# Performance work log

Hardware: AMD Instinct MI355X
Metric: run time of the kernel (lower is better)

The kernel has to match this reference:

```python
import jax, jax.numpy as jnp
import numpy as np
from jax import lax


def _layernorm(x, g, b, eps=1e-5):
    m = x.mean(-1, keepdims=True)
    v = ((x - m) ** 2).mean(-1, keepdims=True)
    return (x - m) * lax.rsqrt(v + eps) * g + b


def _conv1d(x, w, b):
    # x: (B, T, Cin), w: (K, Cin, Cout) -> SAME padding (kernel=3, pad=1)
    y = lax.conv_general_dilated(x, w, (1,), 'SAME',
                                 dimension_numbers=('NWC', 'WIO', 'NWC'))
    return y + b


def _predictor(x, params, mask):
    w1, b1, g1, be1, w2, b2, g2, be2, wl, bl = params
    h = _layernorm(jax.nn.relu(_conv1d(x, w1, b1)), g1, be1)
    h = _layernorm(jax.nn.relu(_conv1d(h, w2, b2)), g2, be2)
    out = (h @ wl)[..., 0] + bl[0]          # (B, T)
    return jnp.where(mask, 0.0, out)


def _length_regulate(x, dur, max_len):
    # vectorized equivalent of the per-token expand/cat/pad loop
    cum = jnp.cumsum(dur, axis=1)            # (B, S)
    mel_len = cum[:, -1]                     # (B,)
    pos = jnp.arange(max_len)                # (T,)
    idx = jax.vmap(lambda c: jnp.searchsorted(c, pos, side='right'))(cum)
    idx = jnp.minimum(idx, x.shape[1] - 1)   # (B, T)
    out = jnp.take_along_axis(x, idx[:, :, None], axis=1)
    valid = (pos[None, :] < mel_len[:, None])[:, :, None]
    return jnp.where(valid, out, 0.0), mel_len


def setup_inputs() -> dict:
    key = jax.random.key(0)
    ks = jax.random.split(key, 12)
    B, S, D, F, K, T, NB = 32, 512, 512, 512, 3, 4096, 256
    inp = {
        'x': jax.random.normal(ks[0], (B, S, D), jnp.float32),
        'src_mask': jnp.zeros((B, S), bool),
        'mel_mask': jnp.zeros((B, T), bool),
        'pitch_truth': jax.random.normal(ks[1], (B, S), jnp.float32),
        'energy_truth': jax.random.normal(ks[2], (B, S), jnp.float32),
        'duration_truth': jax.random.randint(ks[3], (B, S), 0, 8, jnp.int32),
        'conv1_w': 0.05 * jax.random.normal(ks[4], (3, K, D, F), jnp.float32),
        'conv1_b': jnp.zeros((3, F), jnp.float32),
        'ln1_g': jnp.ones((3, F), jnp.float32),
        'ln1_b': jnp.zeros((3, F), jnp.float32),
        'conv2_w': 0.05 * jax.random.normal(ks[5], (3, K, F, F), jnp.float32),
        'conv2_b': jnp.zeros((3, F), jnp.float32),
        'ln2_g': jnp.ones((3, F), jnp.float32),
        'ln2_b': jnp.zeros((3, F), jnp.float32),
        'lin_w': 0.05 * jax.random.normal(ks[6], (3, F, 1), jnp.float32),
        'lin_b': jnp.zeros((3, 1), jnp.float32),
        'pitch_emb': 0.05 * jax.random.normal(ks[7], (NB, D), jnp.float32),
        'energy_emb': 0.05 * jax.random.normal(ks[8], (NB, D), jnp.float32),
        'pitch_bins': jnp.linspace(-3.0, 3.0, NB - 1),
        'energy_bins': jnp.linspace(-3.0, 3.0, NB - 1),
        'max_mel_len': T,
    }
    return inp


def reference(x, src_mask, mel_mask, pitch_truth, energy_truth, duration_truth,
              conv1_w, conv1_b, ln1_g, ln1_b, conv2_w, conv2_b, ln2_g, ln2_b,
              lin_w, lin_b, pitch_emb, energy_emb, pitch_bins, energy_bins,
              max_mel_len):
    def params(i):
        return (conv1_w[i], conv1_b[i], ln1_g[i], ln1_b[i],
                conv2_w[i], conv2_b[i], ln2_g[i], ln2_b[i], lin_w[i], lin_b[i])

    # pitch (predictor idx 0)
    pitch_pred = _predictor(x, params(0), src_mask)
    x = x + pitch_emb[jnp.searchsorted(pitch_bins, pitch_truth, side='left')]
    # energy (idx 1)
    energy_pred = _predictor(x, params(1), src_mask)
    x = x + energy_emb[jnp.searchsorted(energy_bins, energy_truth, side='left')]
    # duration (idx 2)
    log_dur = _predictor(x, params(2), src_mask)
    # length regulation with ground-truth durations (training path)
    x_out, mel_len = _length_regulate(x, duration_truth, max_mel_len)
    return x_out, pitch_pred, energy_pred, log_dur, mel_len, mel_mask
```

## Files before the change

### kernel.cpp

```cpp
#include <hip/hip_runtime.h>
#include <hip/hip_bf16.h>


#define B_ 32
#define S_ 512
#define D_ 512
#define F_ 512
#define T_ 4096
#define SP_ 514
#define KK_ 1536
#define NITER 12
#define SLOT ((size_t)B_ * SP_ * D_)

typedef __attribute__((ext_vector_type(8))) short bf16x8;
typedef __attribute__((ext_vector_type(4))) float f32x4;

__device__ __forceinline__ float bf2f(unsigned short u) {
  union { unsigned int i; float f; } c; c.i = (unsigned int)u << 16; return c.f;
}
__device__ __forceinline__ unsigned short f2bf(float f) {
  __hip_bfloat16 h = __float2bfloat16(f);
  return *(unsigned short*)&h;
}

struct Job {
  const __hip_bfloat16* Pin;
  const __hip_bfloat16* WT;
  const float* bias;
  const float* g;
  const float* be;
  const float* wl;
  const float* bl;
  const unsigned char* mask;
  __hip_bfloat16* Pout;
  float* pred;
  int mode;
};

#define WT_BLKS 1152
#define TP_BLKS 8224
__global__ __launch_bounds__(256) void prep_k(const float* __restrict__ x,
                                              const float* __restrict__ W1,
                                              const float* __restrict__ W2,
                                              const int* __restrict__ dur,
                                              const float* __restrict__ ptruth,
                                              const float* __restrict__ pbins,
                                              const float* __restrict__ pemb,
                                              const float* __restrict__ etruth,
                                              const float* __restrict__ ebins,
                                              const float* __restrict__ eemb,
                                              __hip_bfloat16* __restrict__ X0,
                                              __hip_bfloat16* __restrict__ X1,
                                              __hip_bfloat16* __restrict__ X2,
                                              __hip_bfloat16* __restrict__ P0,
                                              __hip_bfloat16* __restrict__ P1,
                                              __hip_bfloat16* __restrict__ WT1,
                                              __hip_bfloat16* __restrict__ WT2,
                                              int* __restrict__ cum,
                                              float* __restrict__ mel_len) {
  const int blk = blockIdx.x;
  const int t = threadIdx.x;
  if (blk < WT_BLKS) {
    __shared__ float tb[64][65];
    const int w = blk / 192;
    const int kt = (blk % 192) >> 3;
    const int ft = blk & 7;
    const float* src = (w < 3) ? (W1 + (size_t)w * KK_ * F_)
                               : (W2 + (size_t)(w - 3) * KK_ * F_);
    __hip_bfloat16* dst = (w < 3) ? (WT1 + (size_t)w * KK_ * F_)
                                  : (WT2 + (size_t)(w - 3) * KK_ * F_);
    const int ty = t >> 4, tx = t & 15;
    #pragma unroll
    for (int j = 0; j < 4; ++j) {
      const int r = ty + j * 16;
      const float4 v = *(const float4*)(src + (size_t)(kt * 64 + r) * F_ + ft * 64 + tx * 4);
      tb[r][tx * 4 + 0] = v.x; tb[r][tx * 4 + 1] = v.y;
      tb[r][tx * 4 + 2] = v.z; tb[r][tx * 4 + 3] = v.w;
    }
    __syncthreads();
    #pragma unroll
    for (int j = 0; j < 4; ++j) {
      const int r = ty + j * 16;
      ushort4 u = make_ushort4(f2bf(tb[tx * 4 + 0][r]), f2bf(tb[tx * 4 + 1][r]),
                               f2bf(tb[tx * 4 + 2][r]), f2bf(tb[tx * 4 + 3][r]));
      *(ushort4*)((unsigned short*)dst + (size_t)(ft * 64 + r) * KK_ + kt * 64 + tx * 4) = u;
    }
  } else if (blk < WT_BLKS + TP_BLKS) {
    __shared__ int i1s[2], i2s[2];
    const int half = t >> 7;
    const int tl = t & 127;
    const int task = (blk - WT_BLKS) * 2 + half;
    if (task < B_ * S_) {
      if (tl == 0) {
        float v = ptruth[task];
        int lo = 0, hi = 255;
        while (lo < hi) { const int mid = (lo + hi) >> 1; if (pbins[mid] < v) lo = mid + 1; else hi = mid; }
        i1s[half] = lo;
        v = etruth[task]; lo = 0; hi = 255;
        while (lo < hi) { const int mid = (lo + hi) >> 1; if (ebins[mid] < v) lo = mid + 1; else hi = mid; }
        i2s[half] = lo;
      }
      __syncthreads();
      const int b = task >> 9, s = task & 511;
      const size_t off = ((size_t)b * SP_ + s + 1) * D_ + tl * 4;
      const float4 v = *(const float4*)(x + (size_t)task * D_ + tl * 4);
      const float4 pe = *(const float4*)(pemb + (size_t)i1s[half] * D_ + tl * 4);
      const float4 ee = *(const float4*)(eemb + (size_t)i2s[half] * D_ + tl * 4);
      *(ushort4*)((unsigned short*)X0 + off) =
          make_ushort4(f2bf(v.x), f2bf(v.y), f2bf(v.z), f2bf(v.w));
      const float4 v1 = make_float4(v.x + pe.x, v.y + pe.y, v.z + pe.z, v.w + pe.w);
      *(ushort4*)((unsigned short*)X1 + off) =
          make_ushort4(f2bf(v1.x), f2bf(v1.y), f2bf(v1.z), f2bf(v1.w));
      *(ushort4*)((unsigned short*)X2 + off) =
          make_ushort4(f2bf(v1.x + ee.x), f2bf(v1.y + ee.y),
                       f2bf(v1.z + ee.z), f2bf(v1.w + ee.w));
    } else {
      __syncthreads();
      const int idx = task - B_ * S_;
      const int b = idx >> 1;
      const int r = (idx & 1) ? (SP_ - 1) : 0;
      const size_t off = ((size_t)b * SP_ + r) * D_ + tl * 4;
      const ushort4 z = make_ushort4(0, 0, 0, 0);
      *(ushort4*)((unsigned short*)X0 + off) = z;
      *(ushort4*)((unsigned short*)X1 + off) = z;
      *(ushort4*)((unsigned short*)X2 + off) = z;
      *(ushort4*)((unsigned short*)P0 + off) = z;
      *(ushort4*)((unsigned short*)P1 + off) = z;
    }
  } else {
    __shared__ int sh[S_];
    const int b = blk - (WT_BLKS + TP_BLKS);
    sh[t] = dur[b * S_ + t];
    sh[t + 256] = dur[b * S_ + t + 256];
    __syncthreads();
    for (int off = 1; off < S_; off <<= 1) {
      const int a1 = (t >= off) ? sh[t - off] : 0;
      const int j2 = t + 256;
      const int a2 = (j2 >= off) ? sh[j2 - off] : 0;
      __syncthreads();
      sh[t] += a1; sh[j2] += a2;
      __syncthreads();
    }
    cum[b * S_ + t] = sh[t];
    cum[b * S_ + t + 256] = sh[t + 256];
    if (t == 255) mel_len[b] = (float)sh[S_ - 1];
  }
}

#define GLOAD(gptr, loff) __builtin_amdgcn_global_load_lds(                    \
    (const __attribute__((address_space(1))) void*)(gptr),                     \
    (__attribute__((address_space(3))) void*)(smem + (loff)), 16, 0, 0)

#define PHASE(D, AH, BH, STAGE_STMT, VM_STMT)                                  \
  {                                                                            \
    bf16x8 aR[2][2], bR[2][4];                                                 \
    const char* Ab = smem + (D) * 16384 + (AH) * 8192;                         \
    const char* Bb = smem + 32768 + (D) * 65536 + (BH) * 32768;                \
    _Pragma("unroll")                                                          \
    for (int kh = 0; kh < 2; ++kh) {                                           \
      _Pragma("unroll")                                                        \
      for (int mi = 0; mi < 2; ++mi) {                                         \
        const int row = rowbase + 16 * mi;                                     \
        aR[kh][mi] = *(const bf16x8*)(Ab + row * 128 +                         \
                                      (((kh * 4 + l4) ^ (row & 7)) * 16));     \
      }                                                                        \
      _Pragma("unroll")                                                        \
      for (int ni = 0; ni < 4; ++ni) {                                         \
        const int cl = colbase + 16 * ni;                                      \
        bR[kh][ni] = *(const bf16x8*)(Bb + cl * 128 +                          \
                                      (((kh * 4 + l4) ^ (cl & 7)) * 16));      \
      }                                                                        \
    }                                                                          \
    STAGE_STMT;                                                                \
    __builtin_amdgcn_s_barrier();                                              \
    asm volatile("s_waitcnt lgkmcnt(0)" ::: "memory");                         \
    __builtin_amdgcn_sched_barrier(0);                                         \
    __builtin_amdgcn_s_setprio(1);                                             \
    _Pragma("unroll")                                                          \
    for (int kh = 0; kh < 2; ++kh)                                             \
      _Pragma("unroll")                                                        \
      for (int mi = 0; mi < 2; ++mi)                                           \
        _Pragma("unroll")                                                      \
        for (int ni = 0; ni < 4; ++ni)                                         \
          acc[AH][BH][mi][ni] = __builtin_amdgcn_mfma_f32_16x16x32_bf16(       \
              aR[kh][mi], bR[kh][ni], acc[AH][BH][mi][ni], 0, 0, 0);           \
    __builtin_amdgcn_s_setprio(0);                                             \
    __builtin_amdgcn_sched_barrier(0);                                         \
    VM_STMT;                                                                   \
    __builtin_amdgcn_s_barrier();                                              \
  }

__global__ __launch_bounds__(512, 2) void conv8_k(Job j0, Job j1) {
  extern __shared__ char smem[];
  const Job jb = (blockIdx.x >> 7) ? j1 : j0;
  const int inner = blockIdx.x & 127;
  const int swz = (inner & 7) * 16 + (inner >> 3);
  const int b  = swz >> 2;
  const int st = (swz & 3) * 128;
  const int t = threadIdx.x;
  const int lane = t & 63;
  const int wave = t >> 6;
  const int wm2 = wave >> 2;
  const int wn  = wave & 3;
  const int rA = lane & 15;
  const int l4 = lane >> 4;
  const int rowbase = 32 * wm2 + rA;
  const int colbase = 64 * wn + rA;

  f32x4 acc[2][2][2][4];
  #pragma unroll
  for (int a = 0; a < 2; ++a)
    #pragma unroll
    for (int c = 0; c < 2; ++c)
      #pragma unroll
      for (int m = 0; m < 2; ++m)
        #pragma unroll
        for (int n = 0; n < 4; ++n) acc[a][c][m][n] = (f32x4){0.f, 0.f, 0.f, 0.f};

  auto stageA = [&](int kt, int half) {
    const int r = t >> 3, ch = t & 7;
    const __hip_bfloat16* ga = jb.Pin +
        ((size_t)b * SP_ + st + half * 64 + r + (kt >> 3)) * D_ +
        (kt & 7) * 64 + (ch ^ (r & 7)) * 8;
    GLOAD(ga, (kt & 1) * 16384 + half * 8192 + t * 16);
  };
  auto stageB = [&](int kt, int half) {
    #pragma unroll
    for (int i = 0; i < 4; ++i) {
      const int c = t + i * 512;
      const int fr = c >> 3, ch = c & 7;
      const __hip_bfloat16* gb = jb.WT +
          (size_t)(half * 256 + fr) * KK_ + kt * 64 + (ch ^ (fr & 7)) * 8;
      GLOAD(gb, 32768 + (kt & 1) * 65536 + half * 32768 + c * 16);
    }
  };

  stageA(0, 0); stageB(0, 0); stageA(0, 1); stageB(0, 1);
  stageA(1, 0); stageB(1, 1);
  asm volatile("s_waitcnt vmcnt(5)" ::: "memory");
  __builtin_amdgcn_s_barrier();

  for (int it = 0; it < NITER; ++it) {
    const int tk = 2 * it;
    const bool more = (it < NITER - 1);
    PHASE(0, 0, 0, { stageB(tk + 1, 0); }, );
    PHASE(0, 0, 1, { stageA(tk + 1, 1); }, );
    PHASE(0, 1, 1, { if (more) stageA(tk + 2, 0); }, );
    PHASE(0, 1, 0, { if (more) stageB(tk + 2, 1); },
          if (more) { asm volatile("s_waitcnt vmcnt(5)" ::: "memory"); }
          else      { asm volatile("s_waitcnt vmcnt(0)" ::: "memory"); });
    PHASE(1, 0, 0, { if (more) stageB(tk + 2, 0); }, );
    PHASE(1, 0, 1, { if (more) stageA(tk + 2, 1); }, );
    PHASE(1, 1, 1, { if (more) stageA(tk + 3, 0); }, );
    PHASE(1, 1, 0, { if (more) stageB(tk + 3, 1); },
          if (more) { asm volatile("s_waitcnt vmcnt(5)" ::: "memory"); }
          else      { asm volatile("s_waitcnt vmcnt(0)" ::: "memory"); });
  }

  float* rS = (float*)smem;
  float* rQ = rS + 512;
  float* rP = rQ + 512;
  float* tS = rP + 512;
  float* tQ = tS + 128;
  float* tP = tQ + 128;
  float* wG = tP + 128;
  float* wB = wG + 4;

  const int MODE = jb.mode;
  float bia[2][4], gg[2][4], bb[2][4], ww[2][4];
  #pragma unroll
  for (int bh = 0; bh < 2; ++bh)
    #pragma unroll
    for (int ni = 0; ni < 4; ++ni) {
      const int f = 64 * wn + bh * 256 + 16 * ni + rA;
      bia[bh][ni] = jb.bias[f]; gg[bh][ni] = jb.g[f]; bb[bh][ni] = jb.be[f];
      ww[bh][ni] = (MODE == 1) ? jb.wl[f] : 0.f;
    }
  if (MODE == 1 && wm2 == 0) {
    float gwp = 0.f, bwp = 0.f;
    #pragma unroll
    for (int bh = 0; bh < 2; ++bh)
      #pragma unroll
      for (int ni = 0; ni < 4; ++ni) {
        gwp += gg[bh][ni] * ww[bh][ni]; bwp += bb[bh][ni] * ww[bh][ni];
      }
    #pragma unroll
    for (int o = 1; o < 16; o <<= 1) {
      gwp += __shfl_xor(gwp, o); bwp += __shfl_xor(bwp, o);
    }
    if (lane == 0) { wG[wn] = gwp; wB[wn] = bwp; }
  }
  #pragma unroll
  for (int ah = 0; ah < 2; ++ah)
    #pragma unroll
    for (int mi = 0; mi < 2; ++mi)
      #pragma unroll
      for (int reg = 0; reg < 4; ++reg) {
        float sv = 0.f, sq = 0.f, sp = 0.f;
        #pragma unroll
        for (int bh = 0; bh < 2; ++bh)
          #pragma unroll
          for (int ni = 0; ni < 4; ++ni) {
            float v = fmaxf(acc[ah][bh][mi][ni][reg] + bia[bh][ni], 0.f);
            acc[ah][bh][mi][ni][reg] = v;
            sv += v; sq += v * v;
            sp += v * gg[bh][ni] * ww[bh][ni];
          }
        #pragma unroll
        for (int o = 1; o < 16; o <<= 1) {
          sv += __shfl_xor(sv, o); sq += __shfl_xor(sq, o);
          sp += __shfl_xor(sp, o);
        }
        if (rA == 0) {
          const int lr = 64 * ah + 32 * wm2 + 16 * mi + l4 * 4 + reg;
          rS[wn * 128 + lr] = sv; rQ[wn * 128 + lr] = sq; rP[wn * 128 + lr] = sp;
        }
      }
  __syncthreads();
  if (t < 128) {
    float S = 0.f, Q = 0.f, Pp = 0.f;
    #pragma unroll
    for (int w = 0; w < 4; ++w) {
      S += rS[w * 128 + t]; Q += rQ[w * 128 + t]; Pp += rP[w * 128 + t];
    }
    tS[t] = S; tQ[t] = Q; tP[t] = Pp;
  }
  __syncthreads();
  if (MODE == 0) {
    unsigned short* Pu = (unsigned short*)jb.Pout;
    #pragma unroll
    for (int ah = 0; ah < 2; ++ah)
      #pragma unroll
      for (int mi = 0; mi < 2; ++mi)
        #pragma unroll
        for (int reg = 0; reg < 4; ++reg) {
          const int lr = 64 * ah + 32 * wm2 + 16 * mi + l4 * 4 + reg;
          const float mean = tS[lr] * (1.f / F_);
          const float var = tQ[lr] * (1.f / F_) - mean * mean;
          const float inv = rsqrtf(var + 1e-5f);
          unsigned short* pp = Pu + ((size_t)b * SP_ + st + lr + 1) * D_;
          #pragma unroll
          for (int bh = 0; bh < 2; ++bh)
            #pragma unroll
            for (int ni = 0; ni < 4; ++ni)
              pp[64 * wn + bh * 256 + 16 * ni + rA] =
                  f2bf((acc[ah][bh][mi][ni][reg] - mean) * inv * gg[bh][ni] + bb[bh][ni]);
        }
  } else {
    if (t < 128) {
      const float GW = wG[0] + wG[1] + wG[2] + wG[3];
      const float BW = wB[0] + wB[1] + wB[2] + wB[3];
      const float mean = tS[t] * (1.f / F_);
      const float var = tQ[t] * (1.f / F_) - mean * mean;
      const float inv = rsqrtf(var + 1e-5f);
      const int grow = b * S_ + st + t;
      jb.pred[grow] = jb.mask[grow] ? 0.f
                                    : (inv * tP[t] - inv * mean * GW + BW + jb.bl[0]);
    }
  }
}

__global__ __launch_bounds__(256) void gather_k(const __hip_bfloat16* __restrict__ X,
                                                const int* __restrict__ cum,
                                                const unsigned char* __restrict__ melm,
                                                float* __restrict__ out,
                                                float* __restrict__ maskf) {
  const int b    = blockIdx.x >> 11;
  const int pos0 = (blockIdx.x & 2047) * 2;
  const int half = threadIdx.x >> 7;
  const int tl   = threadIdx.x & 127;
  const int pos  = pos0 + half;
  __shared__ int sidx[2], svalid[2];
  if (tl == 0) {
    const int* c = cum + b * S_;
    int lo = 0, hi = S_;
    while (lo < hi) {
      const int mid = (lo + hi) >> 1;
      if (c[mid] <= pos) lo = mid + 1; else hi = mid;
    }
    sidx[half] = (lo < S_ - 1) ? lo : (S_ - 1);
    svalid[half] = (pos < c[S_ - 1]) ? 1 : 0;
    maskf[(size_t)b * T_ + pos] = melm[(size_t)b * T_ + pos] ? 1.f : 0.f;
  }
  __syncthreads();
  float4 v = make_float4(0.f, 0.f, 0.f, 0.f);
  if (svalid[half]) {
    const ushort4 u = *(const ushort4*)((const unsigned short*)X +
                        ((size_t)b * SP_ + sidx[half] + 1) * D_ + tl * 4);
    v = make_float4(bf2f(u.x), bf2f(u.y), bf2f(u.z), bf2f(u.w));
  }
  *(float4*)(out + ((size_t)b * T_ + pos) * D_ + tl * 4) = v;
}

extern "C" void kernel_launch(void* const* d_in, const int* in_sizes, int n_in,
                              void* d_out, int out_size, void* d_ws, size_t ws_size,
                              hipStream_t stream) {
  const float* x            = (const float*)d_in[0];
  const unsigned char* srcm = (const unsigned char*)d_in[1];
  const unsigned char* melm = (const unsigned char*)d_in[2];
  const float* pitch_truth  = (const float*)d_in[3];
  const float* energy_truth = (const float*)d_in[4];
  const int*   dur          = (const int*)d_in[5];
  const float* conv1_w = (const float*)d_in[6];
  const float* conv1_b = (const float*)d_in[7];
  const float* ln1_g   = (const float*)d_in[8];
  const float* ln1_b   = (const float*)d_in[9];
  const float* conv2_w = (const float*)d_in[10];
  const float* conv2_b = (const float*)d_in[11];
  const float* ln2_g   = (const float*)d_in[12];
  const float* ln2_b   = (const float*)d_in[13];
  const float* lin_w   = (const float*)d_in[14];
  const float* lin_b   = (const float*)d_in[15];
  const float* pitch_emb   = (const float*)d_in[16];
  const float* energy_emb  = (const float*)d_in[17];
  const float* pitch_bins  = (const float*)d_in[18];
  const float* energy_bins = (const float*)d_in[19];

  float* out      = (float*)d_out;
  float* x_out    = out;
  float* p_pitch  = out + (size_t)B_ * T_ * D_;
  float* p_energy = p_pitch + B_ * S_;
  float* p_dur    = p_energy + B_ * S_;
  float* p_mellen = p_dur + B_ * S_;
  float* p_mask   = p_mellen + B_;

  __hip_bfloat16* S0  = (__hip_bfloat16*)d_ws;
  __hip_bfloat16* S1  = S0 + SLOT;
  __hip_bfloat16* S2  = S1 + SLOT;
  __hip_bfloat16* S3  = S2 + SLOT;
  __hip_bfloat16* S4  = S3 + SLOT;
  __hip_bfloat16* WT1 = S4 + SLOT;
  __hip_bfloat16* WT2 = WT1 + (size_t)3 * F_ * KK_;
  int*  cum = (int*)(WT2 + (size_t)3 * F_ * KK_);

  const dim3 blk512t(512), blk256(256);
  const int convLds = 163840;
  hipFuncSetAttribute((const void*)conv8_k,
                      hipFuncAttributeMaxDynamicSharedMemorySize, convLds);

  prep_k<<<dim3(WT_BLKS + TP_BLKS + B_), blk256, 0, stream>>>(
      x, conv1_w, conv2_w, dur, pitch_truth, pitch_bins, pitch_emb,
      energy_truth, energy_bins, energy_emb,
      S0, S1, S2, S3, S4, WT1, WT2, cum, p_mellen);

  auto c1 = [&](int i, const __hip_bfloat16* in, __hip_bfloat16* Pout) {
    return Job{in, WT1 + (size_t)i * F_ * KK_, conv1_b + (size_t)i * F_,
               ln1_g + (size_t)i * F_, ln1_b + (size_t)i * F_,
               nullptr, nullptr, nullptr, Pout, nullptr, 0};
  };
  auto c2 = [&](int i, const __hip_bfloat16* in, float* pred) {
    return Job{in, WT2 + (size_t)i * F_ * KK_, conv2_b + (size_t)i * F_,
               ln2_g + (size_t)i * F_, ln2_b + (size_t)i * F_,
               lin_w + (size_t)i * F_, lin_b + i, srcm, nullptr, pred, 1};
  };

  {
    Job a = c1(0, S0, S3), b = c1(1, S1, S4);
    conv8_k<<<dim3(256), blk512t, convLds, stream>>>(a, b);
  }
  {
    Job a = c2(0, S3, p_pitch), b = c1(2, S2, S0);
    conv8_k<<<dim3(256), blk512t, convLds, stream>>>(a, b);
  }
  {
    Job a = c2(1, S4, p_energy), b = c2(2, S0, p_dur);
    conv8_k<<<dim3(256), blk512t, convLds, stream>>>(a, b);
  }

  gather_k<<<dim3(B_ * T_ / 2), blk256, 0, stream>>>(S2, cum, melm, x_out, p_mask);
}
```

Baseline: 320.2 us.

## Replace phased ping-pong GEMM pipeline with simple double-buffered K loop

Removes the eight-phase PHASE macro schedule, which interleaved half-tile LDS reads, staged global-to-LDS loads and waitcnts, and replaces it with a plain double-buffered loop over 24 K-tiles. Each iteration reads all A and B fragments for the current buffer, issues the full global_load_lds for the next tile, runs 64 MFMAs, then waits vmcnt(0) and barriers. The aim is a simpler schedule with fewer barriers and one sync per K-tile. In exchange it holds many more fragment registers live and waits for each prefetch to fully drain before continuing, so it may overlap memory and compute less well and risks register pressure under launch bounds of 512 threads with 2 blocks.

```diff
diff --git a/kernel.cpp b/kernel.cpp
--- a/kernel.cpp
+++ b/kernel.cpp
@@ -9,7 +9,7 @@
 #define T_ 4096
 #define SP_ 514
 #define KK_ 1536
-#define NITER 12
+#define NKT 24
 #define SLOT ((size_t)B_ * SP_ * D_)
 
 typedef __attribute__((ext_vector_type(8))) short bf16x8;
@@ -151,45 +151,6 @@
     (const __attribute__((address_space(1))) void*)(gptr),                     \
     (__attribute__((address_space(3))) void*)(smem + (loff)), 16, 0, 0)
 
-#define PHASE(D, AH, BH, STAGE_STMT, VM_STMT)                                  \
-  {                                                                            \
-    bf16x8 aR[2][2], bR[2][4];                                                 \
-    const char* Ab = smem + (D) * 16384 + (AH) * 8192;                         \
-    const char* Bb = smem + 32768 + (D) * 65536 + (BH) * 32768;                \
-    _Pragma("unroll")                                                          \
-    for (int kh = 0; kh < 2; ++kh) {                                           \
-      _Pragma("unroll")                                                        \
-      for (int mi = 0; mi < 2; ++mi) {                                         \
-        const int row = rowbase + 16 * mi;                                     \
-        aR[kh][mi] = *(const bf16x8*)(Ab + row * 128 +                         \
-                                      (((kh * 4 + l4) ^ (row & 7)) * 16));     \
-      }                                                                        \
-      _Pragma("unroll")                                                        \
-      for (int ni = 0; ni < 4; ++ni) {                                         \
-        const int cl = colbase + 16 * ni;                                      \
-        bR[kh][ni] = *(const bf16x8*)(Bb + cl * 128 +                          \
-                                      (((kh * 4 + l4) ^ (cl & 7)) * 16));      \
-      }                                                                        \
-    }                                                                          \
-    STAGE_STMT;                                                                \
-    __builtin_amdgcn_s_barrier();                                              \
-    asm volatile("s_waitcnt lgkmcnt(0)" ::: "memory");                         \
-    __builtin_amdgcn_sched_barrier(0);                                         \
-    __builtin_amdgcn_s_setprio(1);                                             \
-    _Pragma("unroll")                                                          \
-    for (int kh = 0; kh < 2; ++kh)                                             \
-      _Pragma("unroll")                                                        \
-      for (int mi = 0; mi < 2; ++mi)                                           \
-        _Pragma("unroll")                                                      \
-        for (int ni = 0; ni < 4; ++ni)                                         \
-          acc[AH][BH][mi][ni] = __builtin_amdgcn_mfma_f32_16x16x32_bf16(       \
-              aR[kh][mi], bR[kh][ni], acc[AH][BH][mi][ni], 0, 0, 0);           \
-    __builtin_amdgcn_s_setprio(0);                                             \
-    __builtin_amdgcn_sched_barrier(0);                                         \
-    VM_STMT;                                                                   \
-    __builtin_amdgcn_s_barrier();                                              \
-  }
-
 __global__ __launch_bounds__(512, 2) void conv8_k(Job j0, Job j1) {
   extern __shared__ char smem[];
   const Job jb = (blockIdx.x >> 7) ? j1 : j0;
@@ -236,25 +197,79 @@
   };
 
   stageA(0, 0); stageB(0, 0); stageA(0, 1); stageB(0, 1);
-  stageA(1, 0); stageB(1, 1);
-  asm volatile("s_waitcnt vmcnt(5)" ::: "memory");
+  asm volatile("s_waitcnt vmcnt(0)" ::: "memory");
   __builtin_amdgcn_s_barrier();
-
-  for (int it = 0; it < NITER; ++it) {
-    const int tk = 2 * it;
-    const bool more = (it < NITER - 1);
-    PHASE(0, 0, 0, { stageB(tk + 1, 0); }, );
-    PHASE(0, 0, 1, { stageA(tk + 1, 1); }, );
-    PHASE(0, 1, 1, { if (more) stageA(tk + 2, 0); }, );
-    PHASE(0, 1, 0, { if (more) stageB(tk + 2, 1); },
-          if (more) { asm volatile("s_waitcnt vmcnt(5)" ::: "memory"); }
-          else      { asm volatile("s_waitcnt vmcnt(0)" ::: "memory"); });
-    PHASE(1, 0, 0, { if (more) stageB(tk + 2, 0); }, );
-    PHASE(1, 0, 1, { if (more) stageA(tk + 2, 1); }, );
-    PHASE(1, 1, 1, { if (more) stageA(tk + 3, 0); }, );
-    PHASE(1, 1, 0, { if (more) stageB(tk + 3, 1); },
-          if (more) { asm volatile("s_waitcnt vmcnt(5)" ::: "memory"); }
-          else      { asm volatile("s_waitcnt vmcnt(0)" ::: "memory"); });
+  __builtin_amdgcn_sched_barrier(0);
+
+  bf16x8 aA[2][2][2];
+  bf16x8 bB0[2][4], bB1[2][4];
+
+  for (int kt = 0; kt < NKT; ++kt) {
+    const int cur = kt & 1;
+    const char* Abase = smem + cur * 16384;
+    const char* Bbase = smem + 32768 + cur * 65536;
+    #pragma unroll
+    for (int ah = 0; ah < 2; ++ah)
+      #pragma unroll
+      for (int kh = 0; kh < 2; ++kh)
+        #pragma unroll
+        for (int mi = 0; mi < 2; ++mi) {
+          const int row = rowbase + 16 * mi;
+          aA[ah][kh][mi] = *(const bf16x8*)(Abase + ah * 8192 + row * 128 +
+                                            (((kh * 4 + l4) ^ (row & 7)) * 16));
+        }
+    #pragma unroll
+    for (int kh = 0; kh < 2; ++kh)
+      #pragma unroll
+      for (int ni = 0; ni < 4; ++ni) {
+        const int cl = colbase + 16 * ni;
+        bB0[kh][ni] = *(const bf16x8*)(Bbase + cl * 128 +
+                                       (((kh * 4 + l4) ^ (cl & 7)) * 16));
+        bB1[kh][ni] = *(const bf16x8*)(Bbase + 32768 + cl * 128 +
+                                       (((kh * 4 + l4) ^ (cl & 7)) * 16));
+      }
+    if (kt < NKT - 1) {
+      stageA(kt + 1, 0); stageB(kt + 1, 0);
+      stageA(kt + 1, 1); stageB(kt + 1, 1);
+    }
+    __builtin_amdgcn_s_setprio(1);
+    #pragma unroll
+    for (int kh = 0; kh < 2; ++kh)
+      #pragma unroll
+      for (int mi = 0; mi < 2; ++mi)
+        #pragma unroll
+        for (int ni = 0; ni < 4; ++ni)
+          acc[0][0][mi][ni] = __builtin_amdgcn_mfma_f32_16x16x32_bf16(
+              aA[0][kh][mi], bB0[kh][ni], acc[0][0][mi][ni], 0, 0, 0);
+    #pragma unroll
+    for (int kh = 0; kh < 2; ++kh)
+      #pragma unroll
+      for (int mi = 0; mi < 2; ++mi)
+        #pragma unroll
+        for (int ni = 0; ni < 4; ++ni)
+          acc[1][0][mi][ni] = __builtin_amdgcn_mfma_f32_16x16x32_bf16(
+              aA[1][kh][mi], bB0[kh][ni], acc[1][0][mi][ni], 0, 0, 0);
+    #pragma unroll
+    for (int kh = 0; kh < 2; ++kh)
+      #pragma unroll
+      for (int mi = 0; mi < 2; ++mi)
+        #pragma unroll
+        for (int ni = 0; ni < 4; ++ni)
+          acc[1][1][mi][ni] = __builtin_amdgcn_mfma_f32_16x16x32_bf16(
+              aA[1][kh][mi], bB1[kh][ni], acc[1][1][mi][ni], 0, 0, 0);
+    #pragma unroll
+    for (int kh = 0; kh < 2; ++kh)
+      #pragma unroll
+      for (int mi = 0; mi < 2; ++mi)
+        #pragma unroll
+        for (int ni = 0; ni < 4; ++ni)
+          acc[0][1][mi][ni] = __builtin_amdgcn_mfma_f32_16x16x32_bf16(
+              aA[0][kh][mi], bB1[kh][ni], acc[0][1][mi][ni], 0, 0, 0);
+    __builtin_amdgcn_s_setprio(0);
+    __builtin_amdgcn_sched_barrier(0);
+    asm volatile("s_waitcnt vmcnt(0)" ::: "memory");
+    __builtin_amdgcn_s_barrier();
+    __builtin_amdgcn_sched_barrier(0);
   }
 
   float* rS = (float*)smem;
```

New measurement: 311.6 us. -2.7%, faster.
